# Performance work log

Hardware: AMD Instinct MI355X
Metric: run time of the kernel (lower is better)

## Reference

```python
import jax, jax.numpy as jnp
import numpy as np

# --- problem dims (see shape_source) ---
B, N0, N1 = 8, 50000, 12500        # batch, fine mesh verts, coarse mesh verts
E = 400000                          # graph edges (avg degree 8)
FIN, C, K, Z = 3, 32, 6, 128        # in feats, conv width, Chebyshev order, latent
DOWN_NNZ = N1 * 4                   # 4 fine verts pooled per coarse vert
UP_NNZ = N0 * 3                     # barycentric upsampling, 3 coarse verts per fine vert


def setup_inputs() -> dict:
    rng = np.random.default_rng(0)
    x = rng.standard_normal((B, N0, FIN)).astype(np.float32)

    # adjacency edges + symmetric-normalized Chebyshev norm (as ChebConv_batch.norm)
    src = rng.integers(0, N0, E)
    dst = rng.integers(0, N0, E)
    edge_index = np.stack([src, dst]).astype(np.int32)
    deg = np.bincount(src, minlength=N0).astype(np.float32)
    dinv = np.where(deg > 0, deg ** -0.5, 0.0).astype(np.float32)
    A_norm = (-dinv[src] * dinv[dst]).astype(np.float32)

    # sparse pooling matrices (row=output vert, col=input vert, val=weight)
    down_row = np.repeat(np.arange(N1), 4)
    down_col = rng.integers(0, N0, DOWN_NNZ)
    down_val = (rng.random(DOWN_NNZ) * 0.25).astype(np.float32)
    up_row = np.repeat(np.arange(N0), 3)
    up_col = rng.integers(0, N1, UP_NNZ)
    up_val = (rng.random(UP_NNZ) / 3.0).astype(np.float32)

    def w(*shape):
        return jnp.asarray((rng.standard_normal(shape) * 0.1).astype(np.float32))

    return {
        "x": jnp.asarray(x),
        "edge_index": jnp.asarray(edge_index),
        "A_norm": jnp.asarray(A_norm),
        "down_idx": jnp.asarray(np.stack([down_row, down_col]).astype(np.int32)),
        "down_val": jnp.asarray(down_val),
        "up_idx": jnp.asarray(np.stack([up_row, up_col]).astype(np.int32)),
        "up_val": jnp.asarray(up_val),
        "W_enc0": w(K, FIN, C), "b_enc0": w(C),
        "W_dec0": w(K, C, C), "b_dec0": w(C),
        "W_dec1": w(K, C, FIN),                      # final conv: bias=None
        "enc_lin_W": w(N1 * C, Z), "enc_lin_b": w(Z),
        "dec_lin_W": w(Z, N1 * C), "dec_lin_b": w(N1 * C),
    }


def _propagate(y, src, dst, norm):
    # y: [B, N, C]; out[:, i] = sum_{e: dst[e]==i} norm[e] * y[:, src[e]]
    m = y[:, src, :] * norm[None, :, None]          # [B, E, C] gather + scale
    return jnp.zeros_like(y).at[:, dst, :].add(m)   # scatter-add


def cheb_conv(x, edge_index, norm, W, b):
    # x: [B, N, Cin]; W: [K, Cin, Cout]; Chebyshev recursion T_k(L~) x
    src, dst = edge_index[0], edge_index[1]
    Tx0 = x
    out = jnp.einsum('bnc,co->bno', Tx0, W[0])
    if W.shape[0] > 1:
        Tx1 = _propagate(x, src, dst, norm)
        out = out + jnp.einsum('bnc,co->bno', Tx1, W[1])
    for k in range(2, W.shape[0]):
        Tx2 = 2.0 * _propagate(Tx1, src, dst, norm) - Tx0
        out = out + jnp.einsum('bnc,co->bno', Tx2, W[k])
        Tx0, Tx1 = Tx1, Tx2
    if b is not None:
        out = out + b
    return out


def surface_pool(x, row, col, val, n_out):
    # out = P @ x per batch, P sparse [n_out, n_in] with (row, col, val)
    m = x[:, col, :] * val[None, :, None]           # [B, nnz, C]
    out = jnp.zeros((x.shape[0], n_out, x.shape[2]), x.dtype)
    return out.at[:, row, :].add(m)


def reference(x, edge_index, A_norm, down_idx, down_val, up_idx, up_val,
              W_enc0, b_enc0, W_dec0, b_dec0, W_dec1,
              enc_lin_W, enc_lin_b, dec_lin_W, dec_lin_b):
    # encoder
    h = jax.nn.relu(cheb_conv(x, edge_index, A_norm, W_enc0, b_enc0))
    h = surface_pool(h, down_idx[0], down_idx[1], down_val, N1)
    z = h.reshape(B, N1 * C) @ enc_lin_W + enc_lin_b
    # decoder
    h = jax.nn.relu(z @ dec_lin_W + dec_lin_b).reshape(B, N1, C)
    h = surface_pool(h, up_idx[0], up_idx[1], up_val, N0)
    h = jax.nn.relu(cheb_conv(h, edge_index, A_norm, W_dec0, b_dec0))
    recon = cheb_conv(h, edge_index, A_norm, W_dec1, None)  # last layer: no bias
    return recon
```

## Files before the change

kernel.cpp:

```cpp
#include <hip/hip_runtime.h>

constexpr int B   = 8;
constexpr int N0  = 50000;
constexpr int N1  = 12500;
constexpr int E   = 400000;
constexpr int FIN = 3;
constexpr int C   = 32;
constexpr int Z   = 128;
constexpr int M   = N1 * C;
constexpr int DOWN_NNZ = N1 * 4;
constexpr int UP_NNZ   = N0 * 3;
constexpr size_t BN4 = (size_t)B * N0 * 4;

__global__ void k_hist(const int* __restrict__ dst, int* __restrict__ cnt) {
    int e = blockIdx.x * 256 + threadIdx.x;
    if (e < E) atomicAdd(&cnt[dst[e]], 1);
}

__global__ void k_scan_chunk(const int* __restrict__ cnt, int* __restrict__ rp,
                             int* __restrict__ part) {
    __shared__ int s[512];
    int t = threadIdx.x;
    int i = blockIdx.x * 512 + t;
    int v = (i < N0) ? cnt[i] : 0;
    s[t] = v;
    __syncthreads();
    for (int off = 1; off < 512; off <<= 1) {
        int add = (t >= off) ? s[t - off] : 0;
        __syncthreads();
        s[t] += add;
        __syncthreads();
    }
    if (i < N0) rp[i] = s[t] - v;
    if (t == 511) part[blockIdx.x] = s[511];
}

__global__ void k_scan_part(int* part, int nb) {
    if (threadIdx.x == 0 && blockIdx.x == 0) {
        int run = 0;
        for (int c = 0; c < nb; c++) { int t = part[c]; part[c] = run; run += t; }
    }
}

__global__ void k_scan_add(const int* __restrict__ part, int* __restrict__ rp,
                           int* __restrict__ pos) {
    int i = blockIdx.x * 256 + threadIdx.x;
    if (i < N0) {
        int r = rp[i] + part[i >> 9];
        rp[i] = r; pos[i] = r;
        if (i == 0) rp[N0] = E;
    }
}

__global__ void k_scatter(const int* __restrict__ ei, const float* __restrict__ norm,
                          int* __restrict__ pos, int* __restrict__ col_s,
                          float* __restrict__ val_s) {
    int e = blockIdx.x * 256 + threadIdx.x;
    if (e < E) {
        int d = ei[E + e];
        int j = atomicAdd(&pos[d], 1);
        col_s[j] = ei[e];
        val_s[j] = norm[e];
    }
}

template <int SSTR, int USTR, int OSTR, bool HAS_G, bool HAS_SUB, bool SCALE2>
__global__ void k_prop3g(const int* __restrict__ rp, const int* __restrict__ col,
                         const float* __restrict__ val, const float* __restrict__ src,
                         const float* __restrict__ g, const float* __restrict__ sub,
                         float* __restrict__ out) {
    int n = blockIdx.x * 256 + threadIdx.x;
    if (n >= N0) return;
    int b = blockIdx.y;
    const float* sb = src + (size_t)b * N0 * SSTR;
    int s = rp[n], e = rp[n + 1];
    float a0 = 0.f, a1 = 0.f, a2 = 0.f;
    for (int j = s; j < e; j++) {
        int sc = col[j]; float w = val[j];
        if (SSTR == 4) {
            float4 v = *(const float4*)(sb + (size_t)sc * 4);
            a0 += w * v.x; a1 += w * v.y; a2 += w * v.z;
        } else {
            const float* p = sb + (size_t)sc * 3;
            a0 += w * p[0]; a1 += w * p[1]; a2 += w * p[2];
        }
    }
    if (SCALE2) { a0 *= 2.f; a1 *= 2.f; a2 *= 2.f; }
    if (HAS_G) {
        const float* gp = g + ((size_t)b * N0 + n) * 4;
        a0 += gp[0]; a1 += gp[1]; a2 += gp[2];
    }
    if (HAS_SUB) {
        const float* up = sub + ((size_t)b * N0 + n) * USTR;
        a0 -= up[0]; a1 -= up[1]; a2 -= up[2];
    }
    if (OSTR == 4) {
        *(float4*)(out + ((size_t)b * N0 + n) * 4) = make_float4(a0, a1, a2, 0.f);
    } else {
        float* op = out + ((size_t)b * N0 + n) * 3;
        op[0] = a0; op[1] = a1; op[2] = a2;
    }
}

__global__ void k_enc_combine(const float* __restrict__ x,
                              const float* __restrict__ T1, const float* __restrict__ T2,
                              const float* __restrict__ T3, const float* __restrict__ T4,
                              const float* __restrict__ T5,
                              const float* __restrict__ W, const float* __restrict__ bias,
                              float* __restrict__ out) {
    int o = threadIdx.x & 31, nl = threadIdx.x >> 5;
    int n = blockIdx.x * 8 + nl;
    int b = blockIdx.y;
    size_t b3 = ((size_t)b * N0 + n) * 3;
    size_t b4 = ((size_t)b * N0 + n) * 4;
    float t[18];
    t[0] = x[b3 + 0]; t[1] = x[b3 + 1]; t[2] = x[b3 + 2];
    const float* Ts[5] = { T1, T2, T3, T4, T5 };
#pragma unroll
    for (int k = 0; k < 5; k++) {
        t[3 + k * 3 + 0] = Ts[k][b4 + 0];
        t[3 + k * 3 + 1] = Ts[k][b4 + 1];
        t[3 + k * 3 + 2] = Ts[k][b4 + 2];
    }
    float acc = bias[o];
#pragma unroll
    for (int q = 0; q < 18; q++) acc += t[q] * W[q * 32 + o];
    out[((size_t)b * N0 + n) * 32 + o] = fmaxf(acc, 0.f);
}

__global__ void k_pool4(const int* __restrict__ dcol, const float* __restrict__ dval,
                        const float* __restrict__ src, float* __restrict__ out) {
    int c = threadIdx.x & 31, rl = threadIdx.x >> 5;
    int r = blockIdx.x * 8 + rl;
    if (r >= N1) return;
    int b = blockIdx.y;
    const float* sb = src + (size_t)b * N0 * 32;
    float a = 0.f;
#pragma unroll
    for (int t = 0; t < 4; t++) {
        int idx = 4 * r + t;
        a += dval[idx] * sb[(size_t)dcol[idx] * 32 + c];
    }
    out[((size_t)b * N1 + r) * 32 + c] = a;
}

__global__ void k_pool3(const int* __restrict__ ucol, const float* __restrict__ uval,
                        const float* __restrict__ src, float* __restrict__ out) {
    int c = threadIdx.x & 31, rl = threadIdx.x >> 5;
    int i = blockIdx.x * 8 + rl;
    int b = blockIdx.y;
    const float* sb = src + (size_t)b * N1 * 32;
    float a = 0.f;
#pragma unroll
    for (int t = 0; t < 3; t++) {
        int idx = 3 * i + t;
        a += uval[idx] * sb[(size_t)ucol[idx] * 32 + c];
    }
    out[((size_t)b * N0 + i) * 32 + c] = a;
}

__global__ void k_enclin1(const float* __restrict__ S0, const float* __restrict__ W,
                          float* __restrict__ partial) {
    int zl = threadIdx.x & 127, half = threadIdx.x >> 7;
    int m0 = blockIdx.x * 128;
    float acc[B];
#pragma unroll
    for (int b = 0; b < B; b++) acc[b] = 0.f;
    for (int i = 0; i < 64; i++) {
        int m = m0 + half + 2 * i;
        float w = W[(size_t)m * Z + zl];
#pragma unroll
        for (int b = 0; b < B; b++) acc[b] += S0[(size_t)b * M + m] * w;
    }
    __shared__ float red[128 * B];
    if (half == 1) {
#pragma unroll
        for (int b = 0; b < B; b++) red[zl * B + b] = acc[b];
    }
    __syncthreads();
    if (half == 0) {
#pragma unroll
        for (int b = 0; b < B; b++)
            partial[(size_t)blockIdx.x * 1024 + b * 128 + zl] = acc[b] + red[zl * B + b];
    }
}

__global__ void k_enclin2a(const float* __restrict__ partial, float* __restrict__ p2) {
    int i  = blockIdx.x * 256 + threadIdx.x;
    int kc = blockIdx.y;
    int k0 = kc * 125;
    float a = 0.f;
    for (int k = k0; k < k0 + 125; k++) a += partial[(size_t)k * 1024 + i];
    p2[(size_t)kc * 1024 + i] = a;
}

__global__ void k_enclin2b(const float* __restrict__ p2, const float* __restrict__ bias,
                           float* __restrict__ z) {
    int i = blockIdx.x * 256 + threadIdx.x;
    if (i >= B * Z) return;
    float a = bias[i & 127];
#pragma unroll
    for (int k = 0; k < 25; k++) a += p2[(size_t)k * 1024 + i];
    z[i] = a;
}

__global__ void k_declin(const float* __restrict__ z, const float* __restrict__ W,
                         const float* __restrict__ bias, float* __restrict__ out) {
    __shared__ float zs[B * Z];
    for (int i = threadIdx.x; i < B * Z; i += 256) zs[i] = z[i];
    __syncthreads();
    int m = blockIdx.x * 256 + threadIdx.x;
    if (m >= M) return;
    float bv = bias[m];
    float acc[B];
#pragma unroll
    for (int b = 0; b < B; b++) acc[b] = bv;
    for (int j = 0; j < Z; j++) {
        float w = W[(size_t)j * M + m];
#pragma unroll
        for (int b = 0; b < B; b++) acc[b] += zs[b * Z + j] * w;
    }
#pragma unroll
    for (int b = 0; b < B; b++) out[(size_t)b * M + m] = fmaxf(acc[b], 0.f);
}

__global__ void k_conv_init32(const float* __restrict__ in, const float* __restrict__ W,
                              const float* __restrict__ bias, float* __restrict__ out) {
    int lane = threadIdx.x & 31, nl = threadIdx.x >> 5;
    int n = blockIdx.x * 8 + nl;
    float Wr[32];
#pragma unroll
    for (int cc = 0; cc < 32; cc++) Wr[cc] = W[cc * 32 + lane];
    float bv = bias[lane];
#pragma unroll
    for (int b = 0; b < B; b++) {
        size_t base = ((size_t)b * N0 + n) * 32;
        float t = in[base + lane];
        float acc = bv;
#pragma unroll
        for (int cc = 0; cc < 32; cc++) acc += __shfl(t, cc, 32) * Wr[cc];
        out[base + lane] = acc;
    }
}

template <bool HAS_SUB>
__global__ void k_prop_fused32(const int* __restrict__ rp, const int* __restrict__ col,
                               const float* __restrict__ val, const float* __restrict__ src,
                               const float* __restrict__ sub, float* __restrict__ txout,
                               const float* __restrict__ W, float* __restrict__ accb) {
    int lane = threadIdx.x & 31, nl = threadIdx.x >> 5;
    int n = blockIdx.x * 8 + nl;
    int s = rp[n], e = rp[n + 1];
    float a[B];
#pragma unroll
    for (int b = 0; b < B; b++) a[b] = 0.f;
    for (int j = s; j < e; j++) {
        int sc = col[j]; float w = val[j];
        size_t sb = (size_t)sc * 32 + lane;
#pragma unroll
        for (int b = 0; b < B; b++) a[b] += w * src[(size_t)b * N0 * 32 + sb];
    }
    float Wr[32];
#pragma unroll
    for (int cc = 0; cc < 32; cc++) Wr[cc] = W[cc * 32 + lane];
#pragma unroll
    for (int b = 0; b < B; b++) {
        size_t base = ((size_t)b * N0 + n) * 32;
        float t = HAS_SUB ? 2.f * a[b] - sub[base + lane] : a[b];
        txout[base + lane] = t;
        float o = 0.f;
#pragma unroll
        for (int cc = 0; cc < 32; cc++) o += __shfl(t, cc, 32) * Wr[cc];
        accb[base + lane] += o;
    }
}

__global__ void k_proj(const float* __restrict__ ACC, const float* __restrict__ W1,
                       float* __restrict__ G) {
    int lane = threadIdx.x & 31, nl = threadIdx.x >> 5;
    int n = blockIdx.x * 8 + nl;
    int k = (lane < 18) ? lane / 3 : 0;
    int c = (lane < 18) ? lane % 3 : 0;
    float Wr[32];
#pragma unroll
    for (int cc = 0; cc < 32; cc++) Wr[cc] = W1[k * 96 + cc * 3 + c];
#pragma unroll
    for (int b = 0; b < B; b++) {
        float t = fmaxf(ACC[((size_t)b * N0 + n) * 32 + lane], 0.f);
        float o = 0.f;
#pragma unroll
        for (int cc = 0; cc < 32; cc++) o += __shfl(t, cc, 32) * Wr[cc];
        if (lane < 18) G[(size_t)k * BN4 + ((size_t)b * N0 + n) * 4 + c] = o;
    }
}

extern "C" void kernel_launch(void* const* d_in, const int* in_sizes, int n_in,
                              void* d_out, int out_size, void* d_ws, size_t ws_size,
                              hipStream_t stream) {
    const float* x        = (const float*)d_in[0];
    const int*   ei       = (const int*)d_in[1];
    const float* A_norm   = (const float*)d_in[2];
    const int*   down_idx = (const int*)d_in[3];
    const float* down_val = (const float*)d_in[4];
    const int*   up_idx   = (const int*)d_in[5];
    const float* up_val   = (const float*)d_in[6];
    const float* W_enc0   = (const float*)d_in[7];
    const float* b_enc0   = (const float*)d_in[8];
    const float* W_dec0   = (const float*)d_in[9];
    const float* b_dec0   = (const float*)d_in[10];
    const float* W_dec1   = (const float*)d_in[11];
    const float* enc_lin_W = (const float*)d_in[12];
    const float* enc_lin_b = (const float*)d_in[13];
    const float* dec_lin_W = (const float*)d_in[14];
    const float* dec_lin_b = (const float*)d_in[15];
    float* OUT = (float*)d_out;

    char* w8 = (char*)d_ws;
    auto alignup = [](size_t v) { return (v + 255) & ~(size_t)255; };
    size_t off = 0;
    auto carve = [&](size_t bytes) { void* p = w8 + off; off = alignup(off + bytes); return p; };

    int*   row_ptr = (int*)carve((size_t)(N0 + 1) * 4);
    int*   poscnt  = (int*)carve((size_t)N0 * 4);
    int*   part    = (int*)carve(128 * 4);
    int*   col_s   = (int*)carve((size_t)E * 4);
    float* val_s   = (float*)carve((size_t)E * 4);
    float* zbuf    = (float*)carve((size_t)B * Z * 4);
    constexpr size_t BIG = (size_t)B * N0 * C;
    float* A1 = (float*)carve(BIG * 4);
    float* A2 = (float*)carve(BIG * 4);
    float* A3 = (float*)carve(BIG * 4);
    (void)ws_size; (void)n_in; (void)in_sizes; (void)out_size;

    float* T1 = A1 + 0 * BN4;
    float* T2 = A1 + 1 * BN4;
    float* T3 = A1 + 2 * BN4;
    float* T4 = A1 + 3 * BN4;
    float* T5 = A1 + 4 * BN4;
    float* HENC = A2;
    float* S0   = A3;
    float* PART = A2;
    float* P2   = A3 + (size_t)8 * 1024 * 1024;
    float* S1   = A1;
    float* HUP  = A2;
    float* ACC  = A3;
    float* G    = A1;
    float* B4   = A2 + 0 * BN4;
    float* B3   = A2 + 1 * BN4;
    float* B2   = A2 + 2 * BN4;
    float* B1   = A2 + 3 * BN4;

    const int* dcol = down_idx + DOWN_NNZ;
    const int* ucol = up_idx + UP_NNZ;

    dim3 blk(256);
    dim3 gE((E + 255) / 256);
    dim3 gN0t((N0 + 255) / 256);
    dim3 g3(gN0t.x, B);
    dim3 gN8(N0 / 8);
    dim3 gNB(N0 / 8, B);
    dim3 gP4((N1 + 7) / 8, B);
    dim3 gP3(N0 / 8, B);

    hipMemsetAsync(poscnt, 0, (size_t)N0 * 4, stream);
    k_hist<<<gE, blk, 0, stream>>>(ei + E, poscnt);
    int nchunks = (N0 + 511) / 512;
    k_scan_chunk<<<nchunks, 512, 0, stream>>>(poscnt, row_ptr, part);
    k_scan_part<<<1, 1, 0, stream>>>(part, nchunks);
    k_scan_add<<<gN0t, blk, 0, stream>>>(part, row_ptr, poscnt);
    k_scatter<<<gE, blk, 0, stream>>>(ei, A_norm, poscnt, col_s, val_s);

    k_prop3g<3,3,4,false,false,false><<<g3, blk, 0, stream>>>(row_ptr, col_s, val_s, x,  nullptr, nullptr, T1);
    k_prop3g<4,3,4,false,true, true ><<<g3, blk, 0, stream>>>(row_ptr, col_s, val_s, T1, nullptr, x,  T2);
    k_prop3g<4,4,4,false,true, true ><<<g3, blk, 0, stream>>>(row_ptr, col_s, val_s, T2, nullptr, T1, T3);
    k_prop3g<4,4,4,false,true, true ><<<g3, blk, 0, stream>>>(row_ptr, col_s, val_s, T3, nullptr, T2, T4);
    k_prop3g<4,4,4,false,true, true ><<<g3, blk, 0, stream>>>(row_ptr, col_s, val_s, T4, nullptr, T3, T5);
    k_enc_combine<<<gNB, blk, 0, stream>>>(x, T1, T2, T3, T4, T5, W_enc0, b_enc0, HENC);

    k_pool4<<<gP4, blk, 0, stream>>>(dcol, down_val, HENC, S0);

    k_enclin1<<<3125, blk, 0, stream>>>(S0, enc_lin_W, PART);
    dim3 g2a(4, 25);
    k_enclin2a<<<g2a, blk, 0, stream>>>(PART, P2);
    k_enclin2b<<<4, blk, 0, stream>>>(P2, enc_lin_b, zbuf);

    k_declin<<<(M + 255) / 256, blk, 0, stream>>>(zbuf, dec_lin_W, dec_lin_b, S1);

    k_pool3<<<gP3, blk, 0, stream>>>(ucol, up_val, S1, HUP);

    k_conv_init32<<<gN8, blk, 0, stream>>>(HUP, W_dec0, b_dec0, ACC);
    k_prop_fused32<false><<<gN8, blk, 0, stream>>>(row_ptr, col_s, val_s, A2, nullptr, A1, W_dec0 + 1 * C * C, ACC);
    k_prop_fused32<true ><<<gN8, blk, 0, stream>>>(row_ptr, col_s, val_s, A1, A2, A2, W_dec0 + 2 * C * C, ACC);
    k_prop_fused32<true ><<<gN8, blk, 0, stream>>>(row_ptr, col_s, val_s, A2, A1, A1, W_dec0 + 3 * C * C, ACC);
    k_prop_fused32<true ><<<gN8, blk, 0, stream>>>(row_ptr, col_s, val_s, A1, A2, A2, W_dec0 + 4 * C * C, ACC);
    k_prop_fused32<true ><<<gN8, blk, 0, stream>>>(row_ptr, col_s, val_s, A2, A1, A1, W_dec0 + 5 * C * C, ACC);

    k_proj<<<gN8, blk, 0, stream>>>(ACC, W_dec1, G);
    float* G0 = G + 0 * BN4; float* G1 = G + 1 * BN4; float* G2 = G + 2 * BN4;
    float* G3c = G + 3 * BN4; float* G4 = G + 4 * BN4; float* G5 = G + 5 * BN4;
    k_prop3g<4,4,4,true,false,true ><<<g3, blk, 0, stream>>>(row_ptr, col_s, val_s, G5, G4, nullptr, B4);
    k_prop3g<4,4,4,true,true, true ><<<g3, blk, 0, stream>>>(row_ptr, col_s, val_s, B4, G3c, G5, B3);
    k_prop3g<4,4,4,true,true, true ><<<g3, blk, 0, stream>>>(row_ptr, col_s, val_s, B3, G2, B4, B2);
    k_prop3g<4,4,4,true,true, true ><<<g3, blk, 0, stream>>>(row_ptr, col_s, val_s, B2, G1, B3, B1);
    k_prop3g<4,4,3,true,true, false><<<g3, blk, 0, stream>>>(row_ptr, col_s, val_s, B1, G0, B2, OUT);
}
```

Measured before the change: 1.661 ms.

## Interleave batch into block index and fuse upsampling with first decoder conv term

Grids are flattened so consecutive blocks cover the same vertex range across all 8 batches (batch = blockIdx & 7), aiming for better L2 reuse of the CSR row/col/val data and gathered rows. The 32-wide propagation kernel now handles one batch per block instead of looping over 8 batches per warp, which lowers register pressure and raises parallelism but reloads the CSR indices per batch. The up-pooling kernel is fused with the k=0 weight product so the separate init kernel and its re-read of HUP go away. The final Chebyshev step skips writing its unused Tx output.

```diff
diff --git a/kernel.cpp b/kernel.cpp
--- a/kernel.cpp
+++ b/kernel.cpp
@@ -69,9 +69,10 @@
                          const float* __restrict__ val, const float* __restrict__ src,
                          const float* __restrict__ g, const float* __restrict__ sub,
                          float* __restrict__ out) {
-    int n = blockIdx.x * 256 + threadIdx.x;
+    int bid = blockIdx.x;
+    int b = bid & 7;
+    int n = (bid >> 3) * 256 + threadIdx.x;
     if (n >= N0) return;
-    int b = blockIdx.y;
     const float* sb = src + (size_t)b * N0 * SSTR;
     int s = rp[n], e = rp[n + 1];
     float a0 = 0.f, a1 = 0.f, a2 = 0.f;
@@ -130,10 +131,11 @@
 
 __global__ void k_pool4(const int* __restrict__ dcol, const float* __restrict__ dval,
                         const float* __restrict__ src, float* __restrict__ out) {
+    int bid = blockIdx.x;
+    int b = bid & 7;
     int c = threadIdx.x & 31, rl = threadIdx.x >> 5;
-    int r = blockIdx.x * 8 + rl;
+    int r = (bid >> 3) * 8 + rl;
     if (r >= N1) return;
-    int b = blockIdx.y;
     const float* sb = src + (size_t)b * N0 * 32;
     float a = 0.f;
 #pragma unroll
@@ -144,11 +146,14 @@
     out[((size_t)b * N1 + r) * 32 + c] = a;
 }
 
-__global__ void k_pool3(const int* __restrict__ ucol, const float* __restrict__ uval,
-                        const float* __restrict__ src, float* __restrict__ out) {
+__global__ void k_pool3_init(const int* __restrict__ ucol, const float* __restrict__ uval,
+                             const float* __restrict__ src, const float* __restrict__ W,
+                             const float* __restrict__ bias,
+                             float* __restrict__ hup, float* __restrict__ acc) {
+    int bid = blockIdx.x;
+    int b = bid & 7;
     int c = threadIdx.x & 31, rl = threadIdx.x >> 5;
-    int i = blockIdx.x * 8 + rl;
-    int b = blockIdx.y;
+    int i = (bid >> 3) * 8 + rl;
     const float* sb = src + (size_t)b * N1 * 32;
     float a = 0.f;
 #pragma unroll
@@ -156,7 +161,15 @@
         int idx = 3 * i + t;
         a += uval[idx] * sb[(size_t)ucol[idx] * 32 + c];
     }
-    out[((size_t)b * N0 + i) * 32 + c] = a;
+    size_t base = ((size_t)b * N0 + i) * 32;
+    hup[base + c] = a;
+    float Wr[32];
+#pragma unroll
+    for (int cc = 0; cc < 32; cc++) Wr[cc] = W[cc * 32 + c];
+    float o = bias[c];
+#pragma unroll
+    for (int cc = 0; cc < 32; cc++) o += __shfl(a, cc, 32) * Wr[cc];
+    acc[base + c] = o;
 }
 
 __global__ void k_enclin1(const float* __restrict__ S0, const float* __restrict__ W,
@@ -224,55 +237,31 @@
     for (int b = 0; b < B; b++) out[(size_t)b * M + m] = fmaxf(acc[b], 0.f);
 }
 
-__global__ void k_conv_init32(const float* __restrict__ in, const float* __restrict__ W,
-                              const float* __restrict__ bias, float* __restrict__ out) {
-    int lane = threadIdx.x & 31, nl = threadIdx.x >> 5;
-    int n = blockIdx.x * 8 + nl;
-    float Wr[32];
-#pragma unroll
-    for (int cc = 0; cc < 32; cc++) Wr[cc] = W[cc * 32 + lane];
-    float bv = bias[lane];
-#pragma unroll
-    for (int b = 0; b < B; b++) {
-        size_t base = ((size_t)b * N0 + n) * 32;
-        float t = in[base + lane];
-        float acc = bv;
-#pragma unroll
-        for (int cc = 0; cc < 32; cc++) acc += __shfl(t, cc, 32) * Wr[cc];
-        out[base + lane] = acc;
-    }
-}
-
-template <bool HAS_SUB>
+template <bool HAS_SUB, bool WRITE_TX>
 __global__ void k_prop_fused32(const int* __restrict__ rp, const int* __restrict__ col,
                                const float* __restrict__ val, const float* __restrict__ src,
                                const float* __restrict__ sub, float* __restrict__ txout,
                                const float* __restrict__ W, float* __restrict__ accb) {
+    int bid = blockIdx.x;
+    int b = bid & 7;
     int lane = threadIdx.x & 31, nl = threadIdx.x >> 5;
-    int n = blockIdx.x * 8 + nl;
+    int n = (bid >> 3) * 8 + nl;
     int s = rp[n], e = rp[n + 1];
-    float a[B];
-#pragma unroll
-    for (int b = 0; b < B; b++) a[b] = 0.f;
+    const float* sb = src + (size_t)b * N0 * 32;
+    float a = 0.f;
     for (int j = s; j < e; j++) {
-        int sc = col[j]; float w = val[j];
-        size_t sb = (size_t)sc * 32 + lane;
-#pragma unroll
-        for (int b = 0; b < B; b++) a[b] += w * src[(size_t)b * N0 * 32 + sb];
+        a += val[j] * sb[(size_t)col[j] * 32 + lane];
     }
     float Wr[32];
 #pragma unroll
     for (int cc = 0; cc < 32; cc++) Wr[cc] = W[cc * 32 + lane];
-#pragma unroll
-    for (int b = 0; b < B; b++) {
-        size_t base = ((size_t)b * N0 + n) * 32;
-        float t = HAS_SUB ? 2.f * a[b] - sub[base + lane] : a[b];
-        txout[base + lane] = t;
-        float o = 0.f;
-#pragma unroll
-        for (int cc = 0; cc < 32; cc++) o += __shfl(t, cc, 32) * Wr[cc];
-        accb[base + lane] += o;
-    }
+    size_t base = ((size_t)b * N0 + n) * 32;
+    float t = HAS_SUB ? 2.f * a - sub[base + lane] : a;
+    if (WRITE_TX) txout[base + lane] = t;
+    float o = 0.f;
+#pragma unroll
+    for (int cc = 0; cc < 32; cc++) o += __shfl(t, cc, 32) * Wr[cc];
+    accb[base + lane] += o;
 }
 
 __global__ void k_proj(const float* __restrict__ ACC, const float* __restrict__ W1,
@@ -356,11 +345,11 @@
     dim3 blk(256);
     dim3 gE((E + 255) / 256);
     dim3 gN0t((N0 + 255) / 256);
-    dim3 g3(gN0t.x, B);
+    dim3 g3x(((N0 + 255) / 256) * 8);
     dim3 gN8(N0 / 8);
     dim3 gNB(N0 / 8, B);
-    dim3 gP4((N1 + 7) / 8, B);
-    dim3 gP3(N0 / 8, B);
+    dim3 gF(N0);
+    dim3 gP4(((N1 + 7) / 8) * 8);
 
     hipMemsetAsync(poscnt, 0, (size_t)N0 * 4, stream);
     k_hist<<<gE, blk, 0, stream>>>(ei + E, poscnt);
@@ -370,11 +359,11 @@
     k_scan_add<<<gN0t, blk, 0, stream>>>(part, row_ptr, poscnt);
     k_scatter<<<gE, blk, 0, stream>>>(ei, A_norm, poscnt, col_s, val_s);
 
-    k_prop3g<3,3,4,false,false,false><<<g3, blk, 0, stream>>>(row_ptr, col_s, val_s, x,  nullptr, nullptr, T1);
-    k_prop3g<4,3,4,false,true, true ><<<g3, blk, 0, stream>>>(row_ptr, col_s, val_s, T1, nullptr, x,  T2);
-    k_prop3g<4,4,4,false,true, true ><<<g3, blk, 0, stream>>>(row_ptr, col_s, val_s, T2, nullptr, T1, T3);
-    k_prop3g<4,4,4,false,true, true ><<<g3, blk, 0, stream>>>(row_ptr, col_s, val_s, T3, nullptr, T2, T4);
-    k_prop3g<4,4,4,false,true, true ><<<g3, blk, 0, stream>>>(row_ptr, col_s, val_s, T4, nullptr, T3, T5);
+    k_prop3g<3,3,4,false,false,false><<<g3x, blk, 0, stream>>>(row_ptr, col_s, val_s, x,  nullptr, nullptr, T1);
+    k_prop3g<4,3,4,false,true, true ><<<g3x, blk, 0, stream>>>(row_ptr, col_s, val_s, T1, nullptr, x,  T2);
+    k_prop3g<4,4,4,false,true, true ><<<g3x, blk, 0, stream>>>(row_ptr, col_s, val_s, T2, nullptr, T1, T3);
+    k_prop3g<4,4,4,false,true, true ><<<g3x, blk, 0, stream>>>(row_ptr, col_s, val_s, T3, nullptr, T2, T4);
+    k_prop3g<4,4,4,false,true, true ><<<g3x, blk, 0, stream>>>(row_ptr, col_s, val_s, T4, nullptr, T3, T5);
     k_enc_combine<<<gNB, blk, 0, stream>>>(x, T1, T2, T3, T4, T5, W_enc0, b_enc0, HENC);
 
     k_pool4<<<gP4, blk, 0, stream>>>(dcol, down_val, HENC, S0);
@@ -386,21 +375,20 @@
 
     k_declin<<<(M + 255) / 256, blk, 0, stream>>>(zbuf, dec_lin_W, dec_lin_b, S1);
 
-    k_pool3<<<gP3, blk, 0, stream>>>(ucol, up_val, S1, HUP);
-
-    k_conv_init32<<<gN8, blk, 0, stream>>>(HUP, W_dec0, b_dec0, ACC);
-    k_prop_fused32<false><<<gN8, blk, 0, stream>>>(row_ptr, col_s, val_s, A2, nullptr, A1, W_dec0 + 1 * C * C, ACC);
-    k_prop_fused32<true ><<<gN8, blk, 0, stream>>>(row_ptr, col_s, val_s, A1, A2, A2, W_dec0 + 2 * C * C, ACC);
-    k_prop_fused32<true ><<<gN8, blk, 0, stream>>>(row_ptr, col_s, val_s, A2, A1, A1, W_dec0 + 3 * C * C, ACC);
-    k_prop_fused32<true ><<<gN8, blk, 0, stream>>>(row_ptr, col_s, val_s, A1, A2, A2, W_dec0 + 4 * C * C, ACC);
-    k_prop_fused32<true ><<<gN8, blk, 0, stream>>>(row_ptr, col_s, val_s, A2, A1, A1, W_dec0 + 5 * C * C, ACC);
+    k_pool3_init<<<gF, blk, 0, stream>>>(ucol, up_val, S1, W_dec0, b_dec0, HUP, ACC);
+
+    k_prop_fused32<false, true ><<<gF, blk, 0, stream>>>(row_ptr, col_s, val_s, A2, nullptr, A1, W_dec0 + 1 * C * C, ACC);
+    k_prop_fused32<true,  true ><<<gF, blk, 0, stream>>>(row_ptr, col_s, val_s, A1, A2, A2, W_dec0 + 2 * C * C, ACC);
+    k_prop_fused32<true,  true ><<<gF, blk, 0, stream>>>(row_ptr, col_s, val_s, A2, A1, A1, W_dec0 + 3 * C * C, ACC);
+    k_prop_fused32<true,  true ><<<gF, blk, 0, stream>>>(row_ptr, col_s, val_s, A1, A2, A2, W_dec0 + 4 * C * C, ACC);
+    k_prop_fused32<true,  false><<<gF, blk, 0, stream>>>(row_ptr, col_s, val_s, A2, A1, nullptr, W_dec0 + 5 * C * C, ACC);
 
     k_proj<<<gN8, blk, 0, stream>>>(ACC, W_dec1, G);
     float* G0 = G + 0 * BN4; float* G1 = G + 1 * BN4; float* G2 = G + 2 * BN4;
     float* G3c = G + 3 * BN4; float* G4 = G + 4 * BN4; float* G5 = G + 5 * BN4;
-    k_prop3g<4,4,4,true,false,true ><<<g3, blk, 0, stream>>>(row_ptr, col_s, val_s, G5, G4, nullptr, B4);
-    k_prop3g<4,4,4,true,true, true ><<<g3, blk, 0, stream>>>(row_ptr, col_s, val_s, B4, G3c, G5, B3);
-    k_prop3g<4,4,4,true,true, true ><<<g3, blk, 0, stream>>>(row_ptr, col_s, val_s, B3, G2, B4, B2);
-    k_prop3g<4,4,4,true,true, true ><<<g3, blk, 0, stream>>>(row_ptr, col_s, val_s, B2, G1, B3, B1);
-    k_prop3g<4,4,3,true,true, false><<<g3, blk, 0, stream>>>(row_ptr, col_s, val_s, B1, G0, B2, OUT);
-}
+    k_prop3g<4,4,4,true,false,true ><<<g3x, blk, 0, stream>>>(row_ptr, col_s, val_s, G5, G4, nullptr, B4);
+    k_prop3g<4,4,4,true,true, true ><<<g3x, blk, 0, stream>>>(row_ptr, col_s, val_s, B4, G3c, G5, B3);
+    k_prop3g<4,4,4,true,true, true ><<<g3x, blk, 0, stream>>>(row_ptr, col_s, val_s, B3, G2, B4, B2);
+    k_prop3g<4,4,4,true,true, true ><<<g3x, blk, 0, stream>>>(row_ptr, col_s, val_s, B2, G1, B3, B1);
+    k_prop3g<4,4,3,true,true, false><<<g3x, blk, 0, stream>>>(row_ptr, col_s, val_s, B1, G0, B2, OUT);
+}
```

After: 2.056 ms. 23.7% more time.
